# Performance work log

Measured on AMD Instinct MI355X. Metric: run time of the kernel, lower is better.

## Reference

```python
import jax, jax.numpy as jnp
import numpy as np

TOP_K = 2  # num_experts_per_token


def setup_inputs() -> dict:
    key = jax.random.key(0)
    ks = jax.random.split(key, 6)
    B, S, H, F, E = 4, 2048, 1024, 4096, 8  # F = 2 * intermediate_size
    scale = 0.02
    x = jax.random.normal(ks[0], (B, S, H), dtype=jnp.float32)
    gate_w = jax.random.normal(ks[1], (E, H), dtype=jnp.float32) * scale
    w1 = jax.random.normal(ks[2], (E, H, F), dtype=jnp.float32) * scale
    b1 = jnp.zeros((E, F), dtype=jnp.float32)
    w2 = jax.random.normal(ks[3], (E, F, H), dtype=jnp.float32) * scale
    b2 = jnp.zeros((E, H), dtype=jnp.float32)
    return {"x": x, "gate_w": gate_w, "w1": w1, "b1": b1, "w2": w2, "b2": b2}


def reference(x, gate_w, w1, b1, w2, b2):
    # x: [B, S, H]; gate_w: [E, H]; w1: [E, H, F]; b1: [E, F]; w2: [E, F, H]; b2: [E, H]
    E = gate_w.shape[0]
    gate_logits = jnp.einsum('bsh,eh->bse', x, gate_w)
    gate_probs = jax.nn.softmax(gate_logits, axis=-1)
    top_v, top_i = jax.lax.top_k(gate_probs, TOP_K)  # [B, S, K]
    # Combine weight per expert: w[b,s,e] = sum_k top_v[b,s,k] * (top_i[b,s,k] == e)
    onehot = jax.nn.one_hot(top_i, E, dtype=x.dtype)          # [B, S, K, E]
    comb_w = jnp.einsum('bsk,bske->bse', top_v, onehot)       # [B, S, E]
    out = jnp.zeros_like(x)
    for e in range(E):  # small fixed expert loop
        h = jax.nn.silu(jnp.einsum('bsh,hf->bsf', x, w1[e]) + b1[e])
        y = jnp.einsum('bsf,fh->bsh', h, w2[e]) + b2[e]
        out = out + y * comb_w[..., e:e + 1]
    return out
```

## Files before the change

### kernel.cpp

```cpp
#include <hip/hip_runtime.h>
#include <stdint.h>

#define T_TOK 8192
#define HDIM  1024
#define FDIM  4096
#define NEXP  8
#define BT    256
#define RCAP  (2*T_TOK + NEXP*256)
#define LDSB  65536

typedef short  short8  __attribute__((ext_vector_type(8)));
typedef unsigned short ushort8 __attribute__((ext_vector_type(8)));
typedef float  f32x4   __attribute__((ext_vector_type(4)));

#define MFMA __builtin_amdgcn_mfma_f32_16x16x32_bf16

__device__ __forceinline__ unsigned short f2bf(float f) {
  unsigned u = __float_as_uint(f);
  u += 0x7fffu + ((u >> 16) & 1u);
  return (unsigned short)(u >> 16);
}
__device__ __forceinline__ float bf2f(unsigned short u) {
  return __uint_as_float((unsigned)u << 16);
}

__device__ __forceinline__ void gload16(const void* g, void* l) {
  __builtin_amdgcn_global_load_lds(
      (const __attribute__((address_space(1))) void*)g,
      (__attribute__((address_space(3))) void*)l, 16, 0, 0);
}

__device__ __forceinline__ const short8* lds_frag(const char* base, int row, int kbyte) {
  int b = row * 128 + (kbyte ^ ((row & 7) << 4));
  return (const short8*)(base + b);
}

__global__ __launch_bounds__(256) void k_transp_cvt(const float* __restrict__ in,
                                                    unsigned short* __restrict__ out,
                                                    int K, int N) {
  __shared__ unsigned short s[64][72];
  const float* ine = in + (size_t)blockIdx.z * K * N;
  unsigned short* oute = out + (size_t)blockIdx.z * K * N;
  int k0 = blockIdx.y * 64, n0 = blockIdx.x * 64;
  int t = threadIdx.x;
  int kr = t >> 4, nc = (t & 15) * 4;
#pragma unroll
  for (int it = 0; it < 4; ++it) {
    int k = it * 16 + kr;
    float4 v = *(const float4*)(ine + (size_t)(k0 + k) * N + n0 + nc);
    ushort4 u = make_ushort4(f2bf(v.x), f2bf(v.y), f2bf(v.z), f2bf(v.w));
    *(ushort4*)(&s[k][nc]) = u;
  }
  __syncthreads();
  int nr = t >> 3, kc = (t & 7) * 8;
#pragma unroll
  for (int v = 0; v < 2; ++v) {
    int n = v * 32 + nr;
    ushort8 o;
#pragma unroll
    for (int j = 0; j < 8; ++j) o[j] = s[kc + j][n];
    *(ushort8*)(oute + (size_t)(n0 + n) * K + k0 + kc) = o;
  }
}

__global__ void k_gate(const float* __restrict__ x, const float* __restrict__ gw,
                       unsigned short* __restrict__ xb,
                       int2* __restrict__ eidx, float2* __restrict__ ewt) {
  int tid = threadIdx.x;
  int lane = tid & 63;
  int t = blockIdx.x * 4 + (tid >> 6);
  const float* xr = x + (size_t)t * HDIM;
  unsigned short* xbr = xb + (size_t)t * HDIM;
  float acc[NEXP];
#pragma unroll
  for (int e = 0; e < NEXP; e++) acc[e] = 0.f;
#pragma unroll
  for (int i = 0; i < HDIM / 64; i++) {
    float xv = xr[i * 64 + lane];
    xbr[i * 64 + lane] = f2bf(xv);
#pragma unroll
    for (int e = 0; e < NEXP; e++) acc[e] += xv * gw[e * HDIM + i * 64 + lane];
  }
#pragma unroll
  for (int e = 0; e < NEXP; e++) {
    acc[e] += __shfl_xor(acc[e], 32);
    acc[e] += __shfl_xor(acc[e], 16);
    acc[e] += __shfl_xor(acc[e], 8);
    acc[e] += __shfl_xor(acc[e], 4);
    acc[e] += __shfl_xor(acc[e], 2);
    acc[e] += __shfl_xor(acc[e], 1);
  }
  float m = acc[0];
#pragma unroll
  for (int e = 1; e < NEXP; e++) m = fmaxf(m, acc[e]);
  float p[NEXP]; float s = 0.f;
#pragma unroll
  for (int e = 0; e < NEXP; e++) { p[e] = expf(acc[e] - m); s += p[e]; }
  float inv = 1.f / s;
#pragma unroll
  for (int e = 0; e < NEXP; e++) p[e] *= inv;
  int b0 = 0; float v0 = p[0];
#pragma unroll
  for (int e = 1; e < NEXP; e++) if (p[e] > v0) { v0 = p[e]; b0 = e; }
  int b1i = (b0 == 0) ? 1 : 0; float v1 = p[b1i];
#pragma unroll
  for (int e = 0; e < NEXP; e++) if (e != b0 && p[e] > v1) { v1 = p[e]; b1i = e; }
  if (lane == 0) { eidx[t] = make_int2(b0, b1i); ewt[t] = make_float2(v0, v1); }
}

__global__ void k_compact(const int2* __restrict__ eidx,
                          int* __restrict__ list_tok, int* __restrict__ counts) {
  int e = blockIdx.x;
  int tid = threadIdx.x, lane = tid & 63, wid = tid >> 6;
  __shared__ int sbase;
  __shared__ int wcnt[4];
  if (tid == 0) sbase = 0;
  __syncthreads();
  for (int c = 0; c < T_TOK; c += 256) {
    int t = c + tid;
    int2 ei = eidx[t];
    bool sel = (ei.x == e) || (ei.y == e);
    unsigned long long b = __ballot(sel);
    if (lane == 0) wcnt[wid] = __popcll(b);
    __syncthreads();
    int pre = sbase;
    for (int w = 0; w < wid; w++) pre += wcnt[w];
    int pos = pre + __popcll(b & ((1ull << lane) - 1ull));
    if (sel) list_tok[e * T_TOK + pos] = t;
    __syncthreads();
    if (tid == 0) sbase += wcnt[0] + wcnt[1] + wcnt[2] + wcnt[3];
    __syncthreads();
  }
  if (tid == 0) counts[e] = sbase;
}

__global__ void k_offsets(const int* __restrict__ counts, int* __restrict__ off_pad) {
  if (threadIdx.x == 0) {
    int o = 0;
    off_pad[0] = 0;
    for (int e = 0; e < NEXP; e++) {
      o += ((counts[e] + BT - 1) / BT) * BT;
      off_pad[e + 1] = o;
    }
  }
}

__global__ void k_invert(const int* __restrict__ list_tok, const int* __restrict__ counts,
                         const int* __restrict__ off_pad, const int2* __restrict__ eidx,
                         int2* __restrict__ tok2slot) {
  int e = blockIdx.y;
  int p = blockIdx.x * 256 + threadIdx.x;
  if (p < counts[e]) {
    int t = list_tok[e * T_TOK + p];
    int slot = off_pad[e] + p;
    if (eidx[t].x == e) tok2slot[t].x = slot;
    else                tok2slot[t].y = slot;
  }
}

#define STAGE_A(u_, v_) { \
    char* lb_ = smem + (((v_)&1) ? LDSB : 0) + (u_)*16384; \
    gload16(gA[u_][0] + (size_t)(v_)*128, lb_ + dst0); \
    gload16(gA[u_][1] + (size_t)(v_)*128, lb_ + dst1); }
#define STAGE_B(u_, v_) { \
    char* lb_ = smem + (((v_)&1) ? LDSB : 0) + 32768 + (u_)*16384; \
    gload16(gB[u_][0] + (size_t)(v_)*128, lb_ + dst0); \
    gload16(gB[u_][1] + (size_t)(v_)*128, lb_ + dst1); }

#define PHASE(MA, MB, STAGE_STMT, TAIL_STMT) { \
    short8 aA0 = *lds_frag(rdA, (MA)*16 + lr, g16); \
    short8 aA1 = *lds_frag(rdA, (MA)*16 + lr, 64 + g16); \
    short8 aB0 = *lds_frag(rdA, (MB)*16 + lr, g16); \
    short8 aB1 = *lds_frag(rdA, (MB)*16 + lr, 64 + g16); \
    STAGE_STMT; \
    __builtin_amdgcn_s_barrier(); \
    asm volatile("s_waitcnt lgkmcnt(0)" ::: "memory"); \
    __builtin_amdgcn_sched_barrier(0); \
    __builtin_amdgcn_s_setprio(1); \
    acc[MA][0] = MFMA(aA0, b00, acc[MA][0], 0,0,0); acc[MA][0] = MFMA(aA1, b01, acc[MA][0], 0,0,0); \
    acc[MA][1] = MFMA(aA0, b10, acc[MA][1], 0,0,0); acc[MA][1] = MFMA(aA1, b11, acc[MA][1], 0,0,0); \
    acc[MA][2] = MFMA(aA0, b20, acc[MA][2], 0,0,0); acc[MA][2] = MFMA(aA1, b21, acc[MA][2], 0,0,0); \
    acc[MA][3] = MFMA(aA0, b30, acc[MA][3], 0,0,0); acc[MA][3] = MFMA(aA1, b31, acc[MA][3], 0,0,0); \
    acc[MB][0] = MFMA(aB0, b00, acc[MB][0], 0,0,0); acc[MB][0] = MFMA(aB1, b01, acc[MB][0], 0,0,0); \
    acc[MB][1] = MFMA(aB0, b10, acc[MB][1], 0,0,0); acc[MB][1] = MFMA(aB1, b11, acc[MB][1], 0,0,0); \
    acc[MB][2] = MFMA(aB0, b20, acc[MB][2], 0,0,0); acc[MB][2] = MFMA(aB1, b21, acc[MB][2], 0,0,0); \
    acc[MB][3] = MFMA(aB0, b30, acc[MB][3], 0,0,0); acc[MB][3] = MFMA(aB1, b31, acc[MB][3], 0,0,0); \
    __builtin_amdgcn_s_setprio(0); \
    TAIL_STMT; \
    __builtin_amdgcn_s_barrier(); }

#define READ_B4 \
    short8 b00 = *lds_frag(rdB, rb +      lr, g16), b01 = *lds_frag(rdB, rb +      lr, 64 + g16); \
    short8 b10 = *lds_frag(rdB, rb + 16 + lr, g16), b11 = *lds_frag(rdB, rb + 16 + lr, 64 + g16); \
    short8 b20 = *lds_frag(rdB, rb + 32 + lr, g16), b21 = *lds_frag(rdB, rb + 32 + lr, 64 + g16); \
    short8 b30 = *lds_frag(rdB, rb + 48 + lr, g16), b31 = *lds_frag(rdB, rb + 48 + lr, 64 + g16);

#define GEMM_TILE_LOOP(NT) \
  STAGE_A(0,0); STAGE_A(1,0); STAGE_B(0,0); STAGE_B(1,0); STAGE_B(0,1); STAGE_B(1,1); \
  asm volatile("s_waitcnt vmcnt(4)" ::: "memory"); \
  __builtin_amdgcn_s_barrier(); \
  for (int v = 0; v < (NT); ++v) { \
    const char* rdA = smem + ((v&1) ? LDSB : 0) + wm * 16384; \
    const char* rdB = smem + ((v&1) ? LDSB : 0) + 32768 + (wn >> 1) * 16384; \
    int rb = (wn & 1) * 64; \
    READ_B4; \
    PHASE(0, 1, { if (v+1 < (NT)) STAGE_A(0, v+1); }, {}); \
    PHASE(2, 3, { if (v+1 < (NT)) STAGE_A(1, v+1); }, {}); \
    PHASE(4, 5, { if (v+2 < (NT)) STAGE_B(0, v+2); }, {}); \
    PHASE(6, 7, { if (v+2 < (NT)) STAGE_B(1, v+2); }, { \
      if (v+2 < (NT))      { asm volatile("s_waitcnt vmcnt(4)" ::: "memory"); } \
      else if (v+1 < (NT)) { asm volatile("s_waitcnt vmcnt(0)" ::: "memory"); } }); \
  }

__global__ __launch_bounds__(512, 2) void k_gemm1(
    const unsigned short* __restrict__ xb, const unsigned short* __restrict__ w1t,
    const float* __restrict__ b1, const int* __restrict__ list_tok,
    const int* __restrict__ counts, const int* __restrict__ off_pad,
    unsigned short* __restrict__ h) {
  extern __shared__ char smem[];
  int i2 = blockIdx.x >> 3;
  int hi = (i2 >= 72) ? 1 : 0;
  int nIdx = ((blockIdx.x & 7) << 1) | hi;
  int mIdx = i2 - hi * 72;
  int r0 = mIdx * BT;
  int n0 = nIdx * BT;
  if (r0 >= off_pad[NEXP]) return;
  int e = 0;
#pragma unroll
  for (int i = 0; i < NEXP; ++i) if (r0 >= off_pad[i + 1]) e = i + 1;
  int base = off_pad[e], cnt = counts[e];

  int t = threadIdx.x, l = t & 63, w = t >> 6;
  int wm = w >> 2, wn = w & 3;
  int lr = l & 15, g16 = (l >> 4) * 16;

  int dst0 = t * 16, dst1 = t * 16 + 8192;
  int srow = t >> 3;
  int skb = (((t & 7) ^ ((t >> 3) & 7)) << 4);
  const char* gA[2][2];
  const char* gB[2][2];
#pragma unroll
  for (int u = 0; u < 2; ++u)
#pragma unroll
    for (int j = 0; j < 2; ++j) {
      int row = u * 128 + srow + 64 * j;
      int se = r0 - base + row;
      int tok = (se < cnt) ? list_tok[e * T_TOK + se] : 0;
      gA[u][j] = (const char*)(xb + (size_t)tok * HDIM) + skb;
      gB[u][j] = (const char*)(w1t + (size_t)e * FDIM * HDIM + (size_t)(n0 + row) * HDIM) + skb;
    }

  f32x4 acc[8][4];
#pragma unroll
  for (int m = 0; m < 8; ++m)
#pragma unroll
    for (int n = 0; n < 4; ++n) acc[m][n] = (f32x4){0.f, 0.f, 0.f, 0.f};

  GEMM_TILE_LOOP(HDIM / 64);

  const float* b1e = b1 + (size_t)e * FDIM + n0;
  unsigned short* Cs = (unsigned short*)smem;
  int lh = l >> 4, lh4 = lh * 4;
  int cswz = lh << 4;
#pragma unroll
  for (int n = 0; n < 4; ++n) {
    int col = wn * 64 + n * 16 + lr;
    int colX = col ^ cswz;
    float bv = b1e[col];
#pragma unroll
    for (int m = 0; m < 8; ++m) {
      int row = wm * 128 + m * 16 + lh4;
#pragma unroll
      for (int i = 0; i < 4; ++i) {
        float vv = acc[m][n][i] + bv;
        Cs[(size_t)(row + i) * BT + colX] = f2bf(vv / (1.f + __expf(-vv)));
      }
    }
  }
  __syncthreads();
#pragma unroll
  for (int s = 0; s < 16; ++s) {
    int lin = s * 512 + t;
    int row = lin >> 5, c8 = (lin & 31) * 8;
    int c8X = c8 ^ (((row >> 2) & 3) << 4);
    *(ushort8*)(h + (size_t)(r0 + row) * FDIM + n0 + c8) = *(const ushort8*)(Cs + (size_t)row * BT + c8X);
  }
}

__global__ __launch_bounds__(512, 2) void k_gemm2(
    const unsigned short* __restrict__ h, const unsigned short* __restrict__ w2t,
    const float* __restrict__ b2, const int* __restrict__ off_pad,
    unsigned short* __restrict__ ypartA, unsigned short* __restrict__ ypartB) {
  extern __shared__ char smem[];
  int nz = blockIdx.x & 7;
  int mIdx = blockIdx.x >> 3;
  int r0 = mIdx * BT;
  int n0 = (nz >> 1) * BT;
  int z  = nz & 1;
  if (r0 >= off_pad[NEXP]) return;
  int e = 0;
#pragma unroll
  for (int i = 0; i < NEXP; ++i) if (r0 >= off_pad[i + 1]) e = i + 1;

  int t = threadIdx.x, l = t & 63, w = t >> 6;
  int wm = w >> 2, wn = w & 3;
  int lr = l & 15, g16 = (l >> 4) * 16;

  int dst0 = t * 16, dst1 = t * 16 + 8192;
  int srow = t >> 3;
  int skb = (((t & 7) ^ ((t >> 3) & 7)) << 4);
  const char* gA[2][2];
  const char* gB[2][2];
#pragma unroll
  for (int u = 0; u < 2; ++u)
#pragma unroll
    for (int j = 0; j < 2; ++j) {
      int row = u * 128 + srow + 64 * j;
      gA[u][j] = (const char*)(h + (size_t)(r0 + row) * FDIM + (size_t)z * 2048) + skb;
      gB[u][j] = (const char*)(w2t + (size_t)e * HDIM * FDIM + (size_t)(n0 + row) * FDIM + (size_t)z * 2048) + skb;
    }

  f32x4 acc[8][4];
#pragma unroll
  for (int m = 0; m < 8; ++m)
#pragma unroll
    for (int n = 0; n < 4; ++n) acc[m][n] = (f32x4){0.f, 0.f, 0.f, 0.f};

  GEMM_TILE_LOOP(2048 / 64);

  const float* b2e = b2 + (size_t)e * HDIM + n0;
  unsigned short* yp = z ? ypartB : ypartA;
  unsigned short* Cs = (unsigned short*)smem;
  int lh = l >> 4, lh4 = lh * 4;
  int cswz = lh << 4;
#pragma unroll
  for (int n = 0; n < 4; ++n) {
    int col = wn * 64 + n * 16 + lr;
    int colX = col ^ cswz;
    float bv = (z == 0) ? b2e[col] : 0.f;
#pragma unroll
    for (int m = 0; m < 8; ++m) {
      int row = wm * 128 + m * 16 + lh4;
#pragma unroll
      for (int i = 0; i < 4; ++i)
        Cs[(size_t)(row + i) * BT + colX] = f2bf(acc[m][n][i] + bv);
    }
  }
  __syncthreads();
#pragma unroll
  for (int s = 0; s < 16; ++s) {
    int lin = s * 512 + t;
    int row = lin >> 5, c8 = (lin & 31) * 8;
    int c8X = c8 ^ (((row >> 2) & 3) << 4);
    *(ushort8*)(yp + (size_t)(r0 + row) * HDIM + n0 + c8) = *(const ushort8*)(Cs + (size_t)row * BT + c8X);
  }
}

__global__ void k_reduce(const unsigned short* __restrict__ ypartA,
                         const unsigned short* __restrict__ ypartB,
                         const int2* __restrict__ tok2slot, const float2* __restrict__ ewt,
                         float* __restrict__ out) {
  int idx = blockIdx.x * 256 + threadIdx.x;
  int t = idx >> 7;
  int c8 = (idx & 127) * 8;
  int2 s = tok2slot[t];
  float2 wv = ewt[t];
  ushort8 a0 = *(const ushort8*)(ypartA + (size_t)s.x * HDIM + c8);
  ushort8 a1 = *(const ushort8*)(ypartB + (size_t)s.x * HDIM + c8);
  ushort8 b0 = *(const ushort8*)(ypartA + (size_t)s.y * HDIM + c8);
  ushort8 b1 = *(const ushort8*)(ypartB + (size_t)s.y * HDIM + c8);
  float o[8];
#pragma unroll
  for (int j = 0; j < 8; ++j)
    o[j] = wv.x * (bf2f((unsigned short)a0[j]) + bf2f((unsigned short)a1[j]))
         + wv.y * (bf2f((unsigned short)b0[j]) + bf2f((unsigned short)b1[j]));
  float* op = out + (size_t)t * HDIM + c8;
  *(float4*)op = make_float4(o[0], o[1], o[2], o[3]);
  *(float4*)(op + 4) = make_float4(o[4], o[5], o[6], o[7]);
}

extern "C" void kernel_launch(void* const* d_in, const int* in_sizes, int n_in,
                              void* d_out, int out_size, void* d_ws, size_t ws_size,
                              hipStream_t stream) {
  const float* x  = (const float*)d_in[0];
  const float* gw = (const float*)d_in[1];
  const float* w1 = (const float*)d_in[2];
  const float* b1 = (const float*)d_in[3];
  const float* w2 = (const float*)d_in[4];
  const float* b2 = (const float*)d_in[5];
  float* out = (float*)d_out;

  char* ws = (char*)d_ws;
  size_t off = 0;
  unsigned short* xb = (unsigned short*)(ws + off); off += (size_t)T_TOK * HDIM * 2;
  int2*   eidx = (int2*)(ws + off);   off += (size_t)T_TOK * 8;
  float2* ewt  = (float2*)(ws + off); off += (size_t)T_TOK * 8;
  int2* tok2slot = (int2*)(ws + off); off += (size_t)T_TOK * 8;
  int*  list_tok = (int*)(ws + off);  off += (size_t)NEXP * T_TOK * 4;
  int* counts  = (int*)(ws + off); off += 64;
  int* off_pad = (int*)(ws + off); off += 64;
  off = (off + 255) & ~(size_t)255;
  unsigned short* h      = (unsigned short*)(ws + off); off += (size_t)RCAP * FDIM * 2;
  unsigned short* wT     = (unsigned short*)(ws + off); off += (size_t)NEXP * HDIM * FDIM * 2;
  unsigned short* ypartA = (unsigned short*)(ws + off); off += (size_t)RCAP * HDIM * 2;
  unsigned short* ypartB = (unsigned short*)(ws + off); off += (size_t)RCAP * HDIM * 2;
  if (ws_size < off) return;

  hipFuncSetAttribute((const void*)k_gemm1, hipFuncAttributeMaxDynamicSharedMemorySize, 131072);
  hipFuncSetAttribute((const void*)k_gemm2, hipFuncAttributeMaxDynamicSharedMemorySize, 131072);

  k_gate<<<T_TOK / 4, 256, 0, stream>>>(x, gw, xb, eidx, ewt);
  k_compact<<<NEXP, 256, 0, stream>>>(eidx, list_tok, counts);
  k_offsets<<<1, 64, 0, stream>>>(counts, off_pad);
  k_invert<<<dim3(T_TOK / 256, NEXP), 256, 0, stream>>>(list_tok, counts, off_pad, eidx, tok2slot);
  k_transp_cvt<<<dim3(FDIM / 64, HDIM / 64, NEXP), 256, 0, stream>>>(w1, wT, HDIM, FDIM);
  k_gemm1<<<8 * 144, 512, 131072, stream>>>(xb, wT, b1, list_tok, counts, off_pad, h);
  k_transp_cvt<<<dim3(HDIM / 64, FDIM / 64, NEXP), 256, 0, stream>>>(w2, wT, FDIM, HDIM);
  k_gemm2<<<8 * 72, 512, 131072, stream>>>(h, wT, b2, off_pad, ypartA, ypartB);
  k_reduce<<<T_TOK * (HDIM / 8) / 256, 256, 0, stream>>>(ypartA, ypartB, tok2slot, ewt, out);
}
```

Baseline: 523.5 us.

## Switch expert GEMMs from 16x16x32 to 32x32x16 bf16 MFMA tiles

Replaces the 16x16x32 MFMA instruction with 32x32x16 in both expert GEMM kernels. Each wave now holds a 4x2 grid of 32x32 accumulators and issues fewer, larger MFMAs per k-step. The per-tile schedule is restructured into two phases: all A stages are issued in the first, all B stages in the second. The epilogue store swizzle is remapped for the new accumulator layout, and SiLU now uses a fast reciprocal instead of a division. The larger instruction reuses each loaded LDS fragment across more math, lowering LDS read traffic per FLOP, but it changes register pressure and the overlap between loads and compute.

```diff
diff --git a/kernel.cpp b/kernel.cpp
--- a/kernel.cpp
+++ b/kernel.cpp
@@ -11,9 +11,9 @@
 
 typedef short  short8  __attribute__((ext_vector_type(8)));
 typedef unsigned short ushort8 __attribute__((ext_vector_type(8)));
-typedef float  f32x4   __attribute__((ext_vector_type(4)));
-
-#define MFMA __builtin_amdgcn_mfma_f32_16x16x32_bf16
+typedef float  f32x16  __attribute__((ext_vector_type(16)));
+
+#define MFMA32 __builtin_amdgcn_mfma_f32_32x32x16_bf16
 
 __device__ __forceinline__ unsigned short f2bf(float f) {
   unsigned u = __float_as_uint(f);
@@ -167,35 +167,45 @@
     gload16(gB[u_][0] + (size_t)(v_)*128, lb_ + dst0); \
     gload16(gB[u_][1] + (size_t)(v_)*128, lb_ + dst1); }
 
-#define PHASE(MA, MB, STAGE_STMT, TAIL_STMT) { \
-    short8 aA0 = *lds_frag(rdA, (MA)*16 + lr, g16); \
-    short8 aA1 = *lds_frag(rdA, (MA)*16 + lr, 64 + g16); \
-    short8 aB0 = *lds_frag(rdA, (MB)*16 + lr, g16); \
-    short8 aB1 = *lds_frag(rdA, (MB)*16 + lr, 64 + g16); \
+#define PHASE32(KS0, KS1, STAGE_STMT, TAIL_STMT) { \
+    short8 a0_ = *lds_frag(rdA,      l31, (KS0)*32 + g16h); \
+    short8 a1_ = *lds_frag(rdA, 32 + l31, (KS0)*32 + g16h); \
+    short8 a2_ = *lds_frag(rdA, 64 + l31, (KS0)*32 + g16h); \
+    short8 a3_ = *lds_frag(rdA, 96 + l31, (KS0)*32 + g16h); \
+    short8 a4_ = *lds_frag(rdA,      l31, (KS1)*32 + g16h); \
+    short8 a5_ = *lds_frag(rdA, 32 + l31, (KS1)*32 + g16h); \
+    short8 a6_ = *lds_frag(rdA, 64 + l31, (KS1)*32 + g16h); \
+    short8 a7_ = *lds_frag(rdA, 96 + l31, (KS1)*32 + g16h); \
+    short8 b0_ = *lds_frag(rdB, rb +      l31, (KS0)*32 + g16h); \
+    short8 b1_ = *lds_frag(rdB, rb + 32 + l31, (KS0)*32 + g16h); \
+    short8 b2_ = *lds_frag(rdB, rb +      l31, (KS1)*32 + g16h); \
+    short8 b3_ = *lds_frag(rdB, rb + 32 + l31, (KS1)*32 + g16h); \
     STAGE_STMT; \
     __builtin_amdgcn_s_barrier(); \
     asm volatile("s_waitcnt lgkmcnt(0)" ::: "memory"); \
     __builtin_amdgcn_sched_barrier(0); \
     __builtin_amdgcn_s_setprio(1); \
-    acc[MA][0] = MFMA(aA0, b00, acc[MA][0], 0,0,0); acc[MA][0] = MFMA(aA1, b01, acc[MA][0], 0,0,0); \
-    acc[MA][1] = MFMA(aA0, b10, acc[MA][1], 0,0,0); acc[MA][1] = MFMA(aA1, b11, acc[MA][1], 0,0,0); \
-    acc[MA][2] = MFMA(aA0, b20, acc[MA][2], 0,0,0); acc[MA][2] = MFMA(aA1, b21, acc[MA][2], 0,0,0); \
-    acc[MA][3] = MFMA(aA0, b30, acc[MA][3], 0,0,0); acc[MA][3] = MFMA(aA1, b31, acc[MA][3], 0,0,0); \
-    acc[MB][0] = MFMA(aB0, b00, acc[MB][0], 0,0,0); acc[MB][0] = MFMA(aB1, b01, acc[MB][0], 0,0,0); \
-    acc[MB][1] = MFMA(aB0, b10, acc[MB][1], 0,0,0); acc[MB][1] = MFMA(aB1, b11, acc[MB][1], 0,0,0); \
-    acc[MB][2] = MFMA(aB0, b20, acc[MB][2], 0,0,0); acc[MB][2] = MFMA(aB1, b21, acc[MB][2], 0,0,0); \
-    acc[MB][3] = MFMA(aB0, b30, acc[MB][3], 0,0,0); acc[MB][3] = MFMA(aB1, b31, acc[MB][3], 0,0,0); \
+    acc[0][0] = MFMA32(a0_, b0_, acc[0][0], 0,0,0); \
+    acc[1][0] = MFMA32(a1_, b0_, acc[1][0], 0,0,0); \
+    acc[2][0] = MFMA32(a2_, b0_, acc[2][0], 0,0,0); \
+    acc[3][0] = MFMA32(a3_, b0_, acc[3][0], 0,0,0); \
+    acc[0][1] = MFMA32(a0_, b1_, acc[0][1], 0,0,0); \
+    acc[1][1] = MFMA32(a1_, b1_, acc[1][1], 0,0,0); \
+    acc[2][1] = MFMA32(a2_, b1_, acc[2][1], 0,0,0); \
+    acc[3][1] = MFMA32(a3_, b1_, acc[3][1], 0,0,0); \
+    acc[0][0] = MFMA32(a4_, b2_, acc[0][0], 0,0,0); \
+    acc[1][0] = MFMA32(a5_, b2_, acc[1][0], 0,0,0); \
+    acc[2][0] = MFMA32(a6_, b2_, acc[2][0], 0,0,0); \
+    acc[3][0] = MFMA32(a7_, b2_, acc[3][0], 0,0,0); \
+    acc[0][1] = MFMA32(a4_, b3_, acc[0][1], 0,0,0); \
+    acc[1][1] = MFMA32(a5_, b3_, acc[1][1], 0,0,0); \
+    acc[2][1] = MFMA32(a6_, b3_, acc[2][1], 0,0,0); \
+    acc[3][1] = MFMA32(a7_, b3_, acc[3][1], 0,0,0); \
     __builtin_amdgcn_s_setprio(0); \
     TAIL_STMT; \
     __builtin_amdgcn_s_barrier(); }
 
-#define READ_B4 \
-    short8 b00 = *lds_frag(rdB, rb +      lr, g16), b01 = *lds_frag(rdB, rb +      lr, 64 + g16); \
-    short8 b10 = *lds_frag(rdB, rb + 16 + lr, g16), b11 = *lds_frag(rdB, rb + 16 + lr, 64 + g16); \
-    short8 b20 = *lds_frag(rdB, rb + 32 + lr, g16), b21 = *lds_frag(rdB, rb + 32 + lr, 64 + g16); \
-    short8 b30 = *lds_frag(rdB, rb + 48 + lr, g16), b31 = *lds_frag(rdB, rb + 48 + lr, 64 + g16);
-
-#define GEMM_TILE_LOOP(NT) \
+#define GEMM_TILE_LOOP32(NT) \
   STAGE_A(0,0); STAGE_A(1,0); STAGE_B(0,0); STAGE_B(1,0); STAGE_B(0,1); STAGE_B(1,1); \
   asm volatile("s_waitcnt vmcnt(4)" ::: "memory"); \
   __builtin_amdgcn_s_barrier(); \
@@ -203,12 +213,10 @@
     const char* rdA = smem + ((v&1) ? LDSB : 0) + wm * 16384; \
     const char* rdB = smem + ((v&1) ? LDSB : 0) + 32768 + (wn >> 1) * 16384; \
     int rb = (wn & 1) * 64; \
-    READ_B4; \
-    PHASE(0, 1, { if (v+1 < (NT)) STAGE_A(0, v+1); }, {}); \
-    PHASE(2, 3, { if (v+1 < (NT)) STAGE_A(1, v+1); }, {}); \
-    PHASE(4, 5, { if (v+2 < (NT)) STAGE_B(0, v+2); }, {}); \
-    PHASE(6, 7, { if (v+2 < (NT)) STAGE_B(1, v+2); }, { \
-      if (v+2 < (NT))      { asm volatile("s_waitcnt vmcnt(4)" ::: "memory"); } \
+    PHASE32(0, 1, { if (v+1 < (NT)) { STAGE_A(0, v+1); STAGE_A(1, v+1); } }, {}); \
+    PHASE32(2, 3, {}, { \
+      if (v+2 < (NT)) { STAGE_B(0, v+2); STAGE_B(1, v+2); \
+                        asm volatile("s_waitcnt vmcnt(4)" ::: "memory"); } \
       else if (v+1 < (NT)) { asm volatile("s_waitcnt vmcnt(0)" ::: "memory"); } }); \
   }
 
@@ -232,7 +240,7 @@
 
   int t = threadIdx.x, l = t & 63, w = t >> 6;
   int wm = w >> 2, wn = w & 3;
-  int lr = l & 15, g16 = (l >> 4) * 16;
+  int l31 = l & 31, g16h = (l >> 5) * 16;
 
   int dst0 = t * 16, dst1 = t * 16 + 8192;
   int srow = t >> 3;
@@ -250,30 +258,31 @@
       gB[u][j] = (const char*)(w1t + (size_t)e * FDIM * HDIM + (size_t)(n0 + row) * HDIM) + skb;
     }
 
-  f32x4 acc[8][4];
-#pragma unroll
-  for (int m = 0; m < 8; ++m)
-#pragma unroll
-    for (int n = 0; n < 4; ++n) acc[m][n] = (f32x4){0.f, 0.f, 0.f, 0.f};
-
-  GEMM_TILE_LOOP(HDIM / 64);
+  f32x16 acc[4][2];
+#pragma unroll
+  for (int m = 0; m < 4; ++m)
+#pragma unroll
+    for (int n = 0; n < 2; ++n) acc[m][n] = (f32x16)(0.f);
+
+  GEMM_TILE_LOOP32(HDIM / 64);
 
   const float* b1e = b1 + (size_t)e * FDIM + n0;
   unsigned short* Cs = (unsigned short*)smem;
-  int lh = l >> 4, lh4 = lh * 4;
-  int cswz = lh << 4;
-#pragma unroll
-  for (int n = 0; n < 4; ++n) {
-    int col = wn * 64 + n * 16 + lr;
-    int colX = col ^ cswz;
+  int lhi = l >> 5;
+#pragma unroll
+  for (int nf = 0; nf < 2; ++nf) {
+    int col = wn * 64 + nf * 32 + l31;
+    int colX = col ^ (lhi << 5);
     float bv = b1e[col];
 #pragma unroll
-    for (int m = 0; m < 8; ++m) {
-      int row = wm * 128 + m * 16 + lh4;
-#pragma unroll
-      for (int i = 0; i < 4; ++i) {
-        float vv = acc[m][n][i] + bv;
-        Cs[(size_t)(row + i) * BT + colX] = f2bf(vv / (1.f + __expf(-vv)));
+    for (int mf = 0; mf < 4; ++mf) {
+      int rbase = wm * 128 + mf * 32 + 4 * lhi;
+#pragma unroll
+      for (int r = 0; r < 16; ++r) {
+        int row = rbase + (r & 3) + 8 * (r >> 2);
+        float vv = acc[mf][nf][r] + bv;
+        float sg = __builtin_amdgcn_rcpf(1.f + __expf(-vv));
+        Cs[(size_t)row * BT + colX] = f2bf(vv * sg);
       }
     }
   }
@@ -282,7 +291,7 @@
   for (int s = 0; s < 16; ++s) {
     int lin = s * 512 + t;
     int row = lin >> 5, c8 = (lin & 31) * 8;
-    int c8X = c8 ^ (((row >> 2) & 3) << 4);
+    int c8X = c8 ^ (((row >> 2) & 1) << 5);
     *(ushort8*)(h + (size_t)(r0 + row) * FDIM + n0 + c8) = *(const ushort8*)(Cs + (size_t)row * BT + c8X);
   }
 }
@@ -304,7 +313,7 @@
 
   int t = threadIdx.x, l = t & 63, w = t >> 6;
   int wm = w >> 2, wn = w & 3;
-  int lr = l & 15, g16 = (l >> 4) * 16;
+  int l31 = l & 31, g16h = (l >> 5) * 16;
 
   int dst0 = t * 16, dst1 = t * 16 + 8192;
   int srow = t >> 3;
@@ -320,30 +329,31 @@
       gB[u][j] = (const char*)(w2t + (size_t)e * HDIM * FDIM + (size_t)(n0 + row) * FDIM + (size_t)z * 2048) + skb;
     }
 
-  f32x4 acc[8][4];
-#pragma unroll
-  for (int m = 0; m < 8; ++m)
-#pragma unroll
-    for (int n = 0; n < 4; ++n) acc[m][n] = (f32x4){0.f, 0.f, 0.f, 0.f};
-
-  GEMM_TILE_LOOP(2048 / 64);
+  f32x16 acc[4][2];
+#pragma unroll
+  for (int m = 0; m < 4; ++m)
+#pragma unroll
+    for (int n = 0; n < 2; ++n) acc[m][n] = (f32x16)(0.f);
+
+  GEMM_TILE_LOOP32(2048 / 64);
 
   const float* b2e = b2 + (size_t)e * HDIM + n0;
   unsigned short* yp = z ? ypartB : ypartA;
   unsigned short* Cs = (unsigned short*)smem;
-  int lh = l >> 4, lh4 = lh * 4;
-  int cswz = lh << 4;
-#pragma unroll
-  for (int n = 0; n < 4; ++n) {
-    int col = wn * 64 + n * 16 + lr;
-    int colX = col ^ cswz;
+  int lhi = l >> 5;
+#pragma unroll
+  for (int nf = 0; nf < 2; ++nf) {
+    int col = wn * 64 + nf * 32 + l31;
+    int colX = col ^ (lhi << 5);
     float bv = (z == 0) ? b2e[col] : 0.f;
 #pragma unroll
-    for (int m = 0; m < 8; ++m) {
-      int row = wm * 128 + m * 16 + lh4;
-#pragma unroll
-      for (int i = 0; i < 4; ++i)
-        Cs[(size_t)(row + i) * BT + colX] = f2bf(acc[m][n][i] + bv);
+    for (int mf = 0; mf < 4; ++mf) {
+      int rbase = wm * 128 + mf * 32 + 4 * lhi;
+#pragma unroll
+      for (int r = 0; r < 16; ++r) {
+        int row = rbase + (r & 3) + 8 * (r >> 2);
+        Cs[(size_t)row * BT + colX] = f2bf(acc[mf][nf][r] + bv);
+      }
     }
   }
   __syncthreads();
@@ -351,7 +361,7 @@
   for (int s = 0; s < 16; ++s) {
     int lin = s * 512 + t;
     int row = lin >> 5, c8 = (lin & 31) * 8;
-    int c8X = c8 ^ (((row >> 2) & 3) << 4);
+    int c8X = c8 ^ (((row >> 2) & 1) << 5);
     *(ushort8*)(yp + (size_t)(r0 + row) * HDIM + n0 + c8) = *(const ushort8*)(Cs + (size_t)row * BT + c8X);
   }
 }
```

Result: slower. 558.2 us (+6.6%).

## Remap block indices to XCD-contiguous tiles, precompute LDS offsets, use rcp in SiLU

Applied to the files above, without the earlier changes.

Both GEMM kernels now remap blockIdx so that consecutive work tiles land on the same XCD (blockIdx&7 selects the chunk), aiming at better L2 reuse of expert weights and token rows. The swizzled LDS fragment addresses are precomputed once per thread as base offsets, which removes per-read address arithmetic in the inner loop. The SiLU epilogue swaps a division for a hardware reciprocal approximation, which slightly changes rounding.

```diff
diff --git a/kernel.cpp b/kernel.cpp
--- a/kernel.cpp
+++ b/kernel.cpp
@@ -28,11 +28,6 @@
   __builtin_amdgcn_global_load_lds(
       (const __attribute__((address_space(1))) void*)g,
       (__attribute__((address_space(3))) void*)l, 16, 0, 0);
-}
-
-__device__ __forceinline__ const short8* lds_frag(const char* base, int row, int kbyte) {
-  int b = row * 128 + (kbyte ^ ((row & 7) << 4));
-  return (const short8*)(base + b);
 }
 
 __global__ __launch_bounds__(256) void k_transp_cvt(const float* __restrict__ in,
@@ -168,10 +163,10 @@
     gload16(gB[u_][1] + (size_t)(v_)*128, lb_ + dst1); }
 
 #define PHASE(MA, MB, STAGE_STMT, TAIL_STMT) { \
-    short8 aA0 = *lds_frag(rdA, (MA)*16 + lr, g16); \
-    short8 aA1 = *lds_frag(rdA, (MA)*16 + lr, 64 + g16); \
-    short8 aB0 = *lds_frag(rdA, (MB)*16 + lr, g16); \
-    short8 aB1 = *lds_frag(rdA, (MB)*16 + lr, 64 + g16); \
+    short8 aA0 = *(const short8*)(pA0 + (MA)*2048); \
+    short8 aA1 = *(const short8*)(pA1 + (MA)*2048); \
+    short8 aB0 = *(const short8*)(pA0 + (MB)*2048); \
+    short8 aB1 = *(const short8*)(pA1 + (MB)*2048); \
     STAGE_STMT; \
     __builtin_amdgcn_s_barrier(); \
     asm volatile("s_waitcnt lgkmcnt(0)" ::: "memory"); \
@@ -190,19 +185,21 @@
     __builtin_amdgcn_s_barrier(); }
 
 #define READ_B4 \
-    short8 b00 = *lds_frag(rdB, rb +      lr, g16), b01 = *lds_frag(rdB, rb +      lr, 64 + g16); \
-    short8 b10 = *lds_frag(rdB, rb + 16 + lr, g16), b11 = *lds_frag(rdB, rb + 16 + lr, 64 + g16); \
-    short8 b20 = *lds_frag(rdB, rb + 32 + lr, g16), b21 = *lds_frag(rdB, rb + 32 + lr, 64 + g16); \
-    short8 b30 = *lds_frag(rdB, rb + 48 + lr, g16), b31 = *lds_frag(rdB, rb + 48 + lr, 64 + g16);
+    short8 b00 = *(const short8*)(pB0),        b01 = *(const short8*)(pB1); \
+    short8 b10 = *(const short8*)(pB0 + 2048), b11 = *(const short8*)(pB1 + 2048); \
+    short8 b20 = *(const short8*)(pB0 + 4096), b21 = *(const short8*)(pB1 + 4096); \
+    short8 b30 = *(const short8*)(pB0 + 6144), b31 = *(const short8*)(pB1 + 6144);
 
 #define GEMM_TILE_LOOP(NT) \
   STAGE_A(0,0); STAGE_A(1,0); STAGE_B(0,0); STAGE_B(1,0); STAGE_B(0,1); STAGE_B(1,1); \
   asm volatile("s_waitcnt vmcnt(4)" ::: "memory"); \
   __builtin_amdgcn_s_barrier(); \
   for (int v = 0; v < (NT); ++v) { \
-    const char* rdA = smem + ((v&1) ? LDSB : 0) + wm * 16384; \
-    const char* rdB = smem + ((v&1) ? LDSB : 0) + 32768 + (wn >> 1) * 16384; \
-    int rb = (wn & 1) * 64; \
+    const char* bufb = smem + ((v&1) ? LDSB : 0); \
+    const char* pA0 = bufb + wm * 16384 + aoff0; \
+    const char* pA1 = bufb + wm * 16384 + aoff1; \
+    const char* pB0 = bufb + 32768 + (wn >> 1) * 16384 + boff0; \
+    const char* pB1 = bufb + 32768 + (wn >> 1) * 16384 + boff1; \
     READ_B4; \
     PHASE(0, 1, { if (v+1 < (NT)) STAGE_A(0, v+1); }, {}); \
     PHASE(2, 3, { if (v+1 < (NT)) STAGE_A(1, v+1); }, {}); \
@@ -218,12 +215,9 @@
     const int* __restrict__ counts, const int* __restrict__ off_pad,
     unsigned short* __restrict__ h) {
   extern __shared__ char smem[];
-  int i2 = blockIdx.x >> 3;
-  int hi = (i2 >= 72) ? 1 : 0;
-  int nIdx = ((blockIdx.x & 7) << 1) | hi;
-  int mIdx = i2 - hi * 72;
-  int r0 = mIdx * BT;
-  int n0 = nIdx * BT;
+  int wl = (blockIdx.x & 7) * 144 + (blockIdx.x >> 3);
+  int r0 = (wl >> 4) * BT;
+  int n0 = (wl & 15) * BT;
   if (r0 >= off_pad[NEXP]) return;
   int e = 0;
 #pragma unroll
@@ -233,6 +227,11 @@
   int t = threadIdx.x, l = t & 63, w = t >> 6;
   int wm = w >> 2, wn = w & 3;
   int lr = l & 15, g16 = (l >> 4) * 16;
+  int swz = (lr & 7) << 4;
+  int aoff0 = lr * 128 + (g16 ^ swz);
+  int aoff1 = lr * 128 + ((64 + g16) ^ swz);
+  int boff0 = (wn & 1) * 8192 + aoff0;
+  int boff1 = (wn & 1) * 8192 + aoff1;
 
   int dst0 = t * 16, dst1 = t * 16 + 8192;
   int srow = t >> 3;
@@ -273,7 +272,8 @@
 #pragma unroll
       for (int i = 0; i < 4; ++i) {
         float vv = acc[m][n][i] + bv;
-        Cs[(size_t)(row + i) * BT + colX] = f2bf(vv / (1.f + __expf(-vv)));
+        float sg = __builtin_amdgcn_rcpf(1.f + __expf(-vv));
+        Cs[(size_t)(row + i) * BT + colX] = f2bf(vv * sg);
       }
     }
   }
@@ -292,11 +292,11 @@
     const float* __restrict__ b2, const int* __restrict__ off_pad,
     unsigned short* __restrict__ ypartA, unsigned short* __restrict__ ypartB) {
   extern __shared__ char smem[];
-  int nz = blockIdx.x & 7;
-  int mIdx = blockIdx.x >> 3;
-  int r0 = mIdx * BT;
-  int n0 = (nz >> 1) * BT;
-  int z  = nz & 1;
+  int wl = (blockIdx.x & 7) * 72 + (blockIdx.x >> 3);
+  int mB = wl >> 3, rem = wl & 7;
+  int r0 = mB * BT;
+  int n0 = (rem >> 1) * BT;
+  int z  = rem & 1;
   if (r0 >= off_pad[NEXP]) return;
   int e = 0;
 #pragma unroll
@@ -305,6 +305,11 @@
   int t = threadIdx.x, l = t & 63, w = t >> 6;
   int wm = w >> 2, wn = w & 3;
   int lr = l & 15, g16 = (l >> 4) * 16;
+  int swz = (lr & 7) << 4;
+  int aoff0 = lr * 128 + (g16 ^ swz);
+  int aoff1 = lr * 128 + ((64 + g16) ^ swz);
+  int boff0 = (wn & 1) * 8192 + aoff0;
+  int boff1 = (wn & 1) * 8192 + aoff1;
 
   int dst0 = t * 16, dst1 = t * 16 + 8192;
   int srow = t >> 3;
```

After: 508.1 us. -2.9%, faster.
